# Optimization experiments

Hardware: AMD Instinct MI355X
Metric: run time of the kernel (lower is better)

## Reference

```python
import jax, jax.numpy as jnp
import numpy as np

C_S = 1024
H = 16
M = 1  # num_vector_messages
B, S = 2, 1024
SQRT3 = 3.0 ** 0.5
LN_EPS = 1e-5


def setup_inputs() -> dict:
    key = jax.random.key(0)
    ks = jax.random.split(key, 8)
    s = jax.random.normal(ks[0], (B, S, C_S), dtype=jnp.float32)
    # random proper-ish frames: orthonormalize random 3x3 via QR
    A = jax.random.normal(ks[1], (B, S, 3, 3), dtype=jnp.float32)
    rot, _ = jnp.linalg.qr(A)
    trans = jax.random.normal(ks[2], (B, S, 3), dtype=jnp.float32)
    affine_mask = jnp.ones((B, S), dtype=bool)
    sequence_id = jax.random.randint(ks[3], (B, S), 0, 4, dtype=jnp.int32)
    chain_id = jax.random.randint(ks[4], (B, S), 0, 4, dtype=jnp.int32)
    dim_proj = 4 * H * 3 + H * 3 * M
    ln_w = jnp.ones((C_S,), dtype=jnp.float32)
    w_proj = jax.random.normal(ks[5], (dim_proj, C_S), dtype=jnp.float32) / np.sqrt(C_S)
    w_out = jax.random.normal(ks[6], (C_S, H * 3 * M), dtype=jnp.float32) / np.sqrt(H * 3 * M)
    dist_scale = jnp.zeros((H,), dtype=jnp.float32)
    rot_scale = jnp.zeros((H,), dtype=jnp.float32)
    return {"s": s, "rot": rot, "trans": trans, "ln_w": ln_w, "w_proj": w_proj,
            "w_out": w_out, "dist_scale": dist_scale, "rot_scale": rot_scale,
            "affine_mask": affine_mask, "sequence_id": sequence_id, "chain_id": chain_id}


def reference(s, rot, trans, ln_w, w_proj, w_out, dist_scale, rot_scale,
              affine_mask, sequence_id, chain_id):
    b, n, c = s.shape
    h, m = H, M
    NEG = jnp.finfo(s.dtype).min
    # attention bias: 1.0 for same-sequence pairs, -inf for invalid frames / cross-chain
    seq_eq = (sequence_id[:, :, None] == sequence_id[:, None, :]).astype(s.dtype)
    bias = seq_eq[:, None]  # [b,1,s,s]
    bias = jnp.where(affine_mask[:, None, None, :], bias, NEG)
    chain_diff = chain_id[:, :, None] != chain_id[:, None, :]
    bias = jnp.where(chain_diff[:, None], NEG, bias)
    # LayerNorm (no bias)
    mu = jnp.mean(s, axis=-1, keepdims=True)
    var = jnp.var(s, axis=-1, keepdims=True)
    ns = (s - mu) / jnp.sqrt(var + LN_EPS) * ln_w
    p = jnp.einsum('bsc,dc->bsd', ns, w_proj)
    n_rot = h * 2 * 3 + h * 3 * m
    vec_rot = p[..., :n_rot].reshape(b, n, 2 * h + h * m, 3)
    vec_dist = p[..., n_rot:].reshape(b, n, 2 * h, 3)
    # rotate into global frame; dist vectors also translated
    rot_vecs = jnp.einsum('bsij,bshj->bshi', rot, vec_rot)
    q_rot, k_rot, value = rot_vecs[:, :, :h], rot_vecs[:, :, h:2 * h], rot_vecs[:, :, 2 * h:]
    dist_vecs = jnp.einsum('bsij,bshj->bshi', rot, vec_dist) + trans[:, :, None, :]
    q_dist, k_dist = dist_vecs[:, :, :h], dist_vecs[:, :, h:]
    # distance term [b,h,q,k]
    qd = q_dist.transpose(0, 2, 1, 3)  # b h s 3
    kd = k_dist.transpose(0, 2, 1, 3)
    diff = qd[:, :, :, None, :] - kd[:, :, None, :, :]
    distance_term = jnp.sqrt(jnp.sum(diff * diff, axis=-1)) / SQRT3
    rotation_term = jnp.einsum('bqhd,bkhd->bhqk', q_rot, k_rot) / SQRT3
    dw = jax.nn.softplus(dist_scale)[None, :, None, None]
    rw = jax.nn.softplus(rot_scale)[None, :, None, None]
    attn = rotation_term * rw - distance_term * dw + bias
    attn = jax.nn.softmax(attn, axis=-1)
    # value: b s (h m) 3 -> b h s (m 3)
    v = value.reshape(b, n, h, m, 3).transpose(0, 2, 1, 3, 4).reshape(b, h, n, m * 3)
    out = jnp.einsum('bhqk,bhkd->bhqd', attn, v)
    out = out.reshape(b, h, n, m, 3).transpose(0, 2, 1, 3, 4).reshape(b, n, h * m, 3)
    out = jnp.einsum('bsji,bshj->bshi', rot, out)  # inverse rotation R^T
    out = out.reshape(b, n, h * m * 3)
    out = jnp.where(affine_mask[..., None], out, 0.0)
    return jnp.einsum('bsd,cd->bsc', out, w_out)
```

## Files before the change

kernel.cpp:

```cpp
#include <hip/hip_runtime.h>
#include <math.h>

#define NB 2
#define NS 1024
#define NC 1024
#define NH 16
#define DIMP 240
#define KSPLIT 8
#define AKH 8

constexpr float INV_SQRT3 = 0.57735026919f;

__global__ __launch_bounds__(256) void pre_kernel(const float* __restrict__ s,
                                                  const float* __restrict__ lnw,
                                                  float* __restrict__ ns,
                                                  const float* __restrict__ wp,
                                                  float* __restrict__ wt) {
    __shared__ float sh[64 * 61];
    int tid = threadIdx.x;
    if (blockIdx.x < NB * NS) {
        int row = blockIdx.x;
        const float4* sp = (const float4*)(s + (size_t)row * NC);
        float4 v = sp[tid];
        float sum = v.x + v.y + v.z + v.w;
        float sq  = v.x*v.x + v.y*v.y + v.z*v.z + v.w*v.w;
        #pragma unroll
        for (int off = 32; off; off >>= 1) {
            sum += __shfl_down(sum, off);
            sq  += __shfl_down(sq, off);
        }
        float* s1 = sh; float* s2 = sh + 4;
        int wave = tid >> 6;
        if ((tid & 63) == 0) { s1[wave] = sum; s2[wave] = sq; }
        __syncthreads();
        float tot   = s1[0] + s1[1] + s1[2] + s1[3];
        float totsq = s2[0] + s2[1] + s2[2] + s2[3];
        float mu  = tot * (1.0f / NC);
        float var = totsq * (1.0f / NC) - mu * mu;
        float rstd = rsqrtf(var + 1e-5f);
        float4 w = ((const float4*)lnw)[tid];
        float4 o;
        o.x = (v.x - mu) * rstd * w.x;
        o.y = (v.y - mu) * rstd * w.y;
        o.z = (v.z - mu) * rstd * w.z;
        o.w = (v.w - mu) * rstd * w.w;
        ((float4*)(ns + (size_t)row * NC))[tid] = o;
    } else {
        int bx = blockIdx.x - NB * NS;
        int k0 = (bx & 15) * 64;
        int d0 = (bx >> 4) * 60;
        float (*T)[61] = (float (*)[61])sh;
        #pragma unroll
        for (int i = 0; i < 15; i++) {
            int idx = i * 256 + tid;
            int dd = idx >> 6, kk = idx & 63;
            T[kk][dd] = wp[(size_t)(d0 + dd) * NC + k0 + kk];
        }
        __syncthreads();
        #pragma unroll
        for (int i = 0; i < 15; i++) {
            int idx = i * 256 + tid;
            int kk = idx / 60, dd = idx % 60;
            wt[(size_t)(k0 + kk) * DIMP + d0 + dd] = T[kk][dd];
        }
    }
}

__global__ __launch_bounds__(256) void proj_kernel(const float* __restrict__ ns,
                                                   const float* __restrict__ wt,
                                                   float* __restrict__ pp,
                                                   int use_atomic) {
    int tid = threadIdx.x;
    int wave = tid >> 6, lane = tid & 63;
    int row0 = blockIdx.x * 32;
    int ky = blockIdx.y;
    int k0 = ky * 128;

    __shared__ float A[32][128];
    #pragma unroll
    for (int i = 0; i < 4; i++) {
        int idx = tid + i * 256;
        int r = idx >> 5, c4 = idx & 31;
        *(float4*)&A[r][c4 * 4] = *(const float4*)(ns + (size_t)(row0 + r) * NC + k0 + c4 * 4);
    }
    __syncthreads();

    int wr0 = wave * 8;
    int c0 = lane * 4;
    bool active = c0 < DIMP;
    int c0m = active ? c0 : (DIMP - 4);
    const float* wb = wt + (size_t)k0 * DIMP + c0m;

    float acc[8][4];
    #pragma unroll
    for (int r = 0; r < 8; r++)
        #pragma unroll
        for (int c = 0; c < 4; c++) acc[r][c] = 0.0f;

    float4 wa[4], wx[4];
    #pragma unroll
    for (int j = 0; j < 4; j++) wa[j] = *(const float4*)(wb + (size_t)j * DIMP);

    for (int g = 0; g < 32; g += 2) {
        #pragma unroll
        for (int j = 0; j < 4; j++)
            wx[j] = *(const float4*)(wb + (size_t)((g + 1) * 4 + j) * DIMP);
        #pragma unroll
        for (int r = 0; r < 8; r++) {
            float4 a4 = *(const float4*)&A[wr0 + r][g * 4];
            #pragma unroll
            for (int c = 0; c < 4; c++) {
                float* ac = &acc[r][c];
                *ac = fmaf(a4.x, ((const float*)&wa[0])[c], *ac);
                *ac = fmaf(a4.y, ((const float*)&wa[1])[c], *ac);
                *ac = fmaf(a4.z, ((const float*)&wa[2])[c], *ac);
                *ac = fmaf(a4.w, ((const float*)&wa[3])[c], *ac);
            }
        }
        int kn2 = (g + 2 < 32) ? (g + 2) * 4 : 0;
        #pragma unroll
        for (int j = 0; j < 4; j++)
            wa[j] = *(const float4*)(wb + (size_t)(kn2 + j) * DIMP);
        #pragma unroll
        for (int r = 0; r < 8; r++) {
            float4 a4 = *(const float4*)&A[wr0 + r][(g + 1) * 4];
            #pragma unroll
            for (int c = 0; c < 4; c++) {
                float* ac = &acc[r][c];
                *ac = fmaf(a4.x, ((const float*)&wx[0])[c], *ac);
                *ac = fmaf(a4.y, ((const float*)&wx[1])[c], *ac);
                *ac = fmaf(a4.z, ((const float*)&wx[2])[c], *ac);
                *ac = fmaf(a4.w, ((const float*)&wx[3])[c], *ac);
            }
        }
    }
    if (active) {
        if (use_atomic) {
            #pragma unroll
            for (int r = 0; r < 8; r++)
                #pragma unroll
                for (int c = 0; c < 4; c++)
                    atomicAdd(&pp[(size_t)(row0 + wr0 + r) * DIMP + c0 + c], acc[r][c]);
        } else {
            float* dst = pp + (size_t)ky * (NB * NS * DIMP);
            #pragma unroll
            for (int r = 0; r < 8; r++)
                *(float4*)(dst + (size_t)(row0 + wr0 + r) * DIMP + c0) =
                    make_float4(acc[r][0], acc[r][1], acc[r][2], acc[r][3]);
        }
    }
}

__global__ __launch_bounds__(256) void build_kernel(const float* __restrict__ pp, int nred,
                                                    const float* __restrict__ rot,
                                                    const float* __restrict__ trans,
                                                    const float* __restrict__ dist_scale,
                                                    const float* __restrict__ rot_scale,
                                                    const int* __restrict__ seq,
                                                    const int* __restrict__ chain,
                                                    const int* __restrict__ amask,
                                                    float4* __restrict__ qrb,
                                                    float4* __restrict__ qdb,
                                                    float4* __restrict__ kp) {
    int gid = blockIdx.x * 256 + threadIdx.x;
    if (gid >= NB * NS * 80) return;
    int j  = gid % 80;
    int bs = gid / 80;
    int b  = bs >> 10;
    int si = bs & 1023;
    int off = (j < 48) ? 3 * j : 144 + 3 * (j - 48);
    float vx = 0.0f, vy = 0.0f, vz = 0.0f;
    for (int ky = 0; ky < nred; ky++) {
        const float* pr = pp + (size_t)ky * (NB * NS * DIMP) + (size_t)bs * DIMP + off;
        vx += pr[0]; vy += pr[1]; vz += pr[2];
    }
    const float* R = rot + (size_t)bs * 9;
    float ox = R[0] * vx + R[1] * vy + R[2] * vz;
    float oy = R[3] * vx + R[4] * vy + R[5] * vz;
    float oz = R[6] * vx + R[7] * vy + R[8] * vz;
    if (j >= 48) {
        ox += trans[(size_t)bs * 3 + 0];
        oy += trans[(size_t)bs * 3 + 1];
        oz += trans[(size_t)bs * 3 + 2];
    }
    if (j < 16) {
        float sc = log1pf(__expf(rot_scale[j])) * INV_SQRT3;
        float ck = (float)chain[bs] + 1000.0f * (float)(1 - amask[bs]);
        qrb[(size_t)(b * NH + j) * NS + si] = make_float4(ox * sc, oy * sc, oz * sc, ck);
    } else if (j < 32) {
        int h = j - 16;
        float ck = (float)chain[bs] + 1000.0f * (float)(1 - amask[bs]);
        kp[((size_t)(b * NH + h) * NS + si) * 3 + 0] = make_float4(ox, oy, oz, ck);
    } else if (j < 48) {
        int h = j - 32;
        kp[((size_t)(b * NH + h) * NS + si) * 3 + 2] = make_float4(ox, oy, oz, 0.0f);
    } else if (j < 64) {
        int h = j - 48;
        float sc = log1pf(__expf(dist_scale[h])) * INV_SQRT3;
        qdb[(size_t)(b * NH + h) * NS + si] =
            make_float4(ox * sc, oy * sc, oz * sc, (float)seq[bs]);
    } else {
        int h = j - 64;
        float sc = log1pf(__expf(dist_scale[h])) * INV_SQRT3;
        kp[((size_t)(b * NH + h) * NS + si) * 3 + 1] =
            make_float4(ox * sc, oy * sc, oz * sc, (float)seq[bs]);
    }
}

__global__ __launch_bounds__(256) void attn_kernel(
    const float4* __restrict__ qrb, const float4* __restrict__ qdb,
    const float4* __restrict__ kp,
    float4* __restrict__ pacc) {
    __shared__ float4 kS[384];
    int bx = blockIdx.x;
    int ks = bx & (AKH - 1), qc = (bx >> 3) & 3, bh = bx >> 5;
    int tid = threadIdx.x;
    int q = qc * 256 + tid;
    int base = bh * NS;
    const float4* kb = kp + (size_t)base * 3;

    for (int i = tid; i < 384; i += 256) kS[i] = kb[(size_t)ks * 384 + i];
    __syncthreads();

    float4 a = qrb[base + q];
    float4 d = qdb[base + q];
    float cq = a.w, sq = d.w;

    float l = 0.0f, ax = 0.0f, ay = 0.0f, az = 0.0f;
    #pragma unroll 4
    for (int j = 0; j < 128; j++) {
        float4 f0 = kS[j * 3 + 0];
        float4 f1 = kS[j * 3 + 1];
        float4 f2 = kS[j * 3 + 2];
        float rt = fmaf(a.x, f0.x, fmaf(a.y, f0.y, a.z * f0.z));
        float dx = d.x - f1.x, dy = d.y - f1.y, dz = d.z - f1.z;
        float dist = sqrtf(fmaf(dx, dx, fmaf(dy, dy, dz * dz)));
        float dc = f0.w - cq;
        float arg = fmaf(-100.0f, fabsf(dc), rt - dist) +
                    ((f1.w == sq) ? -15.0f : -16.0f);
        float pw = __expf(arg);
        l += pw;
        ax = fmaf(pw, f2.x, ax);
        ay = fmaf(pw, f2.y, ay);
        az = fmaf(pw, f2.z, az);
    }
    pacc[(size_t)ks * (32 * NS) + base + q] = make_float4(ax, ay, az, l);
}

__global__ __launch_bounds__(256) void attnfin_kernel(const float4* __restrict__ pacc,
                                                      const float4* __restrict__ qrb,
                                                      const float* __restrict__ rot,
                                                      float* __restrict__ small) {
    int i = blockIdx.x * 256 + threadIdx.x;
    int bh = i >> 10, q = i & 1023;
    int b = bh >> 4, h = bh & 15;
    float4 s = make_float4(0.0f, 0.0f, 0.0f, 0.0f);
    #pragma unroll
    for (int j = 0; j < AKH; j++) {
        float4 t = pacc[(size_t)j * (32 * NS) + i];
        s.x += t.x; s.y += t.y; s.z += t.z; s.w += t.w;
    }
    float inv = 1.0f / s.w;
    float ox = s.x * inv, oy = s.y * inv, oz = s.z * inv;
    const float* R = rot + (size_t)(b * NS + q) * 9;
    float wx = R[0] * ox + R[3] * oy + R[6] * oz;
    float wy = R[1] * ox + R[4] * oy + R[7] * oz;
    float wz = R[2] * ox + R[5] * oy + R[8] * oz;
    float cq = qrb[i].w;
    if (cq >= 500.0f) { wx = 0; wy = 0; wz = 0; }
    float* o = small + (size_t)(b * NS + q) * 48 + h * 3;
    o[0] = wx; o[1] = wy; o[2] = wz;
}

__global__ __launch_bounds__(256) void outgemm_kernel(const float* __restrict__ small,
                                                      const float* __restrict__ wout,
                                                      float* __restrict__ out) {
    int c  = blockIdx.y * 256 + threadIdx.x;
    int r0 = blockIdx.x * 16;
    __shared__ float sm[16][48];
    for (int i = threadIdx.x; i < 16 * 48; i += 256)
        sm[i / 48][i % 48] = small[(size_t)(r0 + i / 48) * 48 + i % 48];
    __syncthreads();
    float w[48];
    #pragma unroll
    for (int d = 0; d < 48; d += 4) {
        float4 t = *(const float4*)(wout + (size_t)c * 48 + d);
        w[d] = t.x; w[d + 1] = t.y; w[d + 2] = t.z; w[d + 3] = t.w;
    }
    #pragma unroll 4
    for (int r = 0; r < 16; r++) {
        float acc = 0.0f;
        #pragma unroll
        for (int d = 0; d < 48; d++) acc = fmaf(w[d], sm[r][d], acc);
        out[(size_t)(r0 + r) * NC + c] = acc;
    }
}

extern "C" void kernel_launch(void* const* d_in, const int* in_sizes, int n_in,
                              void* d_out, int out_size, void* d_ws, size_t ws_size,
                              hipStream_t stream) {
    const float* s     = (const float*)d_in[0];
    const float* rot   = (const float*)d_in[1];
    const float* trans = (const float*)d_in[2];
    const float* lnw   = (const float*)d_in[3];
    const float* wproj = (const float*)d_in[4];
    const float* wout  = (const float*)d_in[5];
    const float* dsc   = (const float*)d_in[6];
    const float* rsc   = (const float*)d_in[7];
    const int* amask   = (const int*)d_in[8];
    const int* seq     = (const int*)d_in[9];
    const int* chain   = (const int*)d_in[10];
    float* out = (float*)d_out;

    float* ns = (float*)d_ws;
    float4* qrb = (float4*)(ns + (size_t)NB * NS * NC);
    float4* qdb = qrb + (size_t)NB * NH * NS;
    float4* kpk = qdb + (size_t)NB * NH * NS;
    float* small = (float*)(kpk + (size_t)3 * NB * NH * NS);
    float* pp = small + (size_t)NB * NS * 48;
    float* wt = (float*)qrb;
    float4* pacc = (float4*)pp;

    size_t need = ((char*)(pp + (size_t)KSPLIT * NB * NS * DIMP)) - (char*)d_ws;
    int use_atomic = (ws_size < need) ? 1 : 0;

    pre_kernel<<<NB * NS + 64, 256, 0, stream>>>(s, lnw, ns, wproj, wt);
    if (use_atomic) {
        hipMemsetAsync(pp, 0, (size_t)NB * NS * DIMP * sizeof(float), stream);
        proj_kernel<<<dim3(64, KSPLIT), 256, 0, stream>>>(ns, wt, pp, 1);
        build_kernel<<<(NB * NS * 80 + 255) / 256, 256, 0, stream>>>(pp, 1, rot, trans, dsc, rsc,
                                                                     seq, chain, amask, qrb, qdb, kpk);
    } else {
        proj_kernel<<<dim3(64, KSPLIT), 256, 0, stream>>>(ns, wt, pp, 0);
        build_kernel<<<(NB * NS * 80 + 255) / 256, 256, 0, stream>>>(pp, KSPLIT, rot, trans, dsc, rsc,
                                                                     seq, chain, amask, qrb, qdb, kpk);
    }
    attn_kernel<<<NB * NH * 4 * AKH, 256, 0, stream>>>(qrb, qdb, kpk, pacc);
    attnfin_kernel<<<NB * NH * NS / 256, 256, 0, stream>>>(pacc, qrb, rot, small);
    outgemm_kernel<<<dim3(NB * NS / 16, 4), 256, 0, stream>>>(small, wout, out);
}
```

Baseline: 156.9 us.

## Process two queries per thread in attention and fuse finalize into output GEMM

The attention kernel now handles two query rows per thread, so each key tile loaded into shared memory is reused twice and only half as many blocks are launched. The separate finalize kernel (split-K reduction, normalization, inverse rotation, masking) is merged into the output GEMM, which drops one launch and the intermediate 'small' buffer round trip. The cost is fewer attention blocks (512), which may lower occupancy and latency hiding. The four-fold duplicate finalize work across the blockIdx.y column blocks is also an added cost.

Measured after the change: 163.9 us. +4.5%, slower.

```diff
diff --git a/kernel.cpp b/kernel.cpp
--- a/kernel.cpp
+++ b/kernel.cpp
@@ -213,73 +213,81 @@
     float4* __restrict__ pacc) {
     __shared__ float4 kS[384];
     int bx = blockIdx.x;
-    int ks = bx & (AKH - 1), qc = (bx >> 3) & 3, bh = bx >> 5;
+    int ks = bx & (AKH - 1), qc = (bx >> 3) & 1, bh = bx >> 4;
     int tid = threadIdx.x;
-    int q = qc * 256 + tid;
+    int q1 = qc * 512 + tid;
+    int q2 = q1 + 256;
     int base = bh * NS;
     const float4* kb = kp + (size_t)base * 3;
 
     for (int i = tid; i < 384; i += 256) kS[i] = kb[(size_t)ks * 384 + i];
     __syncthreads();
 
-    float4 a = qrb[base + q];
-    float4 d = qdb[base + q];
-    float cq = a.w, sq = d.w;
-
-    float l = 0.0f, ax = 0.0f, ay = 0.0f, az = 0.0f;
+    float4 a1 = qrb[base + q1], d1 = qdb[base + q1];
+    float4 a2 = qrb[base + q2], d2 = qdb[base + q2];
+    float cq1 = a1.w, sq1 = d1.w, cq2 = a2.w, sq2 = d2.w;
+
+    float l1 = 0, x1 = 0, y1 = 0, z1 = 0;
+    float l2 = 0, x2 = 0, y2 = 0, z2 = 0;
     #pragma unroll 4
     for (int j = 0; j < 128; j++) {
         float4 f0 = kS[j * 3 + 0];
         float4 f1 = kS[j * 3 + 1];
         float4 f2 = kS[j * 3 + 2];
-        float rt = fmaf(a.x, f0.x, fmaf(a.y, f0.y, a.z * f0.z));
-        float dx = d.x - f1.x, dy = d.y - f1.y, dz = d.z - f1.z;
-        float dist = sqrtf(fmaf(dx, dx, fmaf(dy, dy, dz * dz)));
-        float dc = f0.w - cq;
-        float arg = fmaf(-100.0f, fabsf(dc), rt - dist) +
-                    ((f1.w == sq) ? -15.0f : -16.0f);
-        float pw = __expf(arg);
-        l += pw;
-        ax = fmaf(pw, f2.x, ax);
-        ay = fmaf(pw, f2.y, ay);
-        az = fmaf(pw, f2.z, az);
-    }
-    pacc[(size_t)ks * (32 * NS) + base + q] = make_float4(ax, ay, az, l);
-}
-
-__global__ __launch_bounds__(256) void attnfin_kernel(const float4* __restrict__ pacc,
-                                                      const float4* __restrict__ qrb,
-                                                      const float* __restrict__ rot,
-                                                      float* __restrict__ small) {
-    int i = blockIdx.x * 256 + threadIdx.x;
-    int bh = i >> 10, q = i & 1023;
-    int b = bh >> 4, h = bh & 15;
-    float4 s = make_float4(0.0f, 0.0f, 0.0f, 0.0f);
-    #pragma unroll
-    for (int j = 0; j < AKH; j++) {
-        float4 t = pacc[(size_t)j * (32 * NS) + i];
-        s.x += t.x; s.y += t.y; s.z += t.z; s.w += t.w;
-    }
-    float inv = 1.0f / s.w;
-    float ox = s.x * inv, oy = s.y * inv, oz = s.z * inv;
-    const float* R = rot + (size_t)(b * NS + q) * 9;
-    float wx = R[0] * ox + R[3] * oy + R[6] * oz;
-    float wy = R[1] * ox + R[4] * oy + R[7] * oz;
-    float wz = R[2] * ox + R[5] * oy + R[8] * oz;
-    float cq = qrb[i].w;
-    if (cq >= 500.0f) { wx = 0; wy = 0; wz = 0; }
-    float* o = small + (size_t)(b * NS + q) * 48 + h * 3;
-    o[0] = wx; o[1] = wy; o[2] = wz;
-}
-
-__global__ __launch_bounds__(256) void outgemm_kernel(const float* __restrict__ small,
-                                                      const float* __restrict__ wout,
-                                                      float* __restrict__ out) {
-    int c  = blockIdx.y * 256 + threadIdx.x;
+        {
+            float rt = fmaf(a1.x, f0.x, fmaf(a1.y, f0.y, a1.z * f0.z));
+            float dx = d1.x - f1.x, dy = d1.y - f1.y, dz = d1.z - f1.z;
+            float dist = sqrtf(fmaf(dx, dx, fmaf(dy, dy, dz * dz)));
+            float arg = fmaf(-100.0f, fabsf(f0.w - cq1), rt - dist) +
+                        ((f1.w == sq1) ? -15.0f : -16.0f);
+            float pw = __expf(arg);
+            l1 += pw;
+            x1 = fmaf(pw, f2.x, x1); y1 = fmaf(pw, f2.y, y1); z1 = fmaf(pw, f2.z, z1);
+        }
+        {
+            float rt = fmaf(a2.x, f0.x, fmaf(a2.y, f0.y, a2.z * f0.z));
+            float dx = d2.x - f1.x, dy = d2.y - f1.y, dz = d2.z - f1.z;
+            float dist = sqrtf(fmaf(dx, dx, fmaf(dy, dy, dz * dz)));
+            float arg = fmaf(-100.0f, fabsf(f0.w - cq2), rt - dist) +
+                        ((f1.w == sq2) ? -15.0f : -16.0f);
+            float pw = __expf(arg);
+            l2 += pw;
+            x2 = fmaf(pw, f2.x, x2); y2 = fmaf(pw, f2.y, y2); z2 = fmaf(pw, f2.z, z2);
+        }
+    }
+    pacc[(size_t)ks * (32 * NS) + base + q1] = make_float4(x1, y1, z1, l1);
+    pacc[(size_t)ks * (32 * NS) + base + q2] = make_float4(x2, y2, z2, l2);
+}
+
+__global__ __launch_bounds__(256) void finout_kernel(const float4* __restrict__ pacc,
+                                                     const float4* __restrict__ qrb,
+                                                     const float* __restrict__ rot,
+                                                     const float* __restrict__ wout,
+                                                     float* __restrict__ out) {
+    int tid = threadIdx.x;
+    int c  = blockIdx.y * 256 + tid;
     int r0 = blockIdx.x * 16;
     __shared__ float sm[16][48];
-    for (int i = threadIdx.x; i < 16 * 48; i += 256)
-        sm[i / 48][i % 48] = small[(size_t)(r0 + i / 48) * 48 + i % 48];
+    {
+        int r = tid >> 4, h = tid & 15;
+        int row = r0 + r;
+        int b = row >> 10, q = row & 1023;
+        int i = ((b * NH + h) << 10) + q;
+        float4 s4 = make_float4(0.0f, 0.0f, 0.0f, 0.0f);
+        #pragma unroll
+        for (int j = 0; j < AKH; j++) {
+            float4 t = pacc[(size_t)j * (32 * NS) + i];
+            s4.x += t.x; s4.y += t.y; s4.z += t.z; s4.w += t.w;
+        }
+        float inv = 1.0f / s4.w;
+        float ox = s4.x * inv, oy = s4.y * inv, oz = s4.z * inv;
+        const float* R = rot + (size_t)row * 9;
+        float wx = R[0] * ox + R[3] * oy + R[6] * oz;
+        float wy = R[1] * ox + R[4] * oy + R[7] * oz;
+        float wz = R[2] * ox + R[5] * oy + R[8] * oz;
+        if (qrb[i].w >= 500.0f) { wx = 0; wy = 0; wz = 0; }
+        sm[r][h * 3 + 0] = wx; sm[r][h * 3 + 1] = wy; sm[r][h * 3 + 2] = wz;
+    }
     __syncthreads();
     float w[48];
     #pragma unroll
@@ -316,8 +324,7 @@
     float4* qrb = (float4*)(ns + (size_t)NB * NS * NC);
     float4* qdb = qrb + (size_t)NB * NH * NS;
     float4* kpk = qdb + (size_t)NB * NH * NS;
-    float* small = (float*)(kpk + (size_t)3 * NB * NH * NS);
-    float* pp = small + (size_t)NB * NS * 48;
+    float* pp = (float*)(kpk + (size_t)3 * NB * NH * NS);
     float* wt = (float*)qrb;
     float4* pacc = (float4*)pp;
 
@@ -335,7 +342,6 @@
         build_kernel<<<(NB * NS * 80 + 255) / 256, 256, 0, stream>>>(pp, KSPLIT, rot, trans, dsc, rsc,
                                                                      seq, chain, amask, qrb, qdb, kpk);
     }
-    attn_kernel<<<NB * NH * 4 * AKH, 256, 0, stream>>>(qrb, qdb, kpk, pacc);
-    attnfin_kernel<<<NB * NH * NS / 256, 256, 0, stream>>>(pacc, qrb, rot, small);
-    outgemm_kernel<<<dim3(NB * NS / 16, 4), 256, 0, stream>>>(small, wout, out);
-}
+    attn_kernel<<<NB * NH * 2 * AKH, 256, 0, stream>>>(qrb, qdb, kpk, pacc);
+    finout_kernel<<<dim3(NB * NS / 16, 4), 256, 0, stream>>>(pacc, qrb, rot, wout, out);
+}
```
